# Kernel optimization log

Measured on AMD Instinct MI355X. Metric: run time of the kernel, lower is better.

Reference implementation:

```python
import jax, jax.numpy as jnp
import numpy as np

N = 200000  # number of mesh nodes (source hardcodes n; scaled to production)

def setup_inputs() -> dict:
    key = jax.random.key(0)
    ks = jax.random.split(key, 7)
    spatial = jax.random.normal(ks[0], (N, 64), dtype=jnp.float32)
    structural = jax.random.normal(ks[1], (N, 131), dtype=jnp.float32)
    neighbour = jax.random.randint(ks[2], (N, 3), 0, N, dtype=jnp.int64)
    # Conv1d(kernel_size=1) == linear layer; weights [out_c, in_c]
    Wc = jax.random.normal(ks[3], (256, 195), dtype=jnp.float32) * (1.0 / np.sqrt(195))
    bc = jax.random.normal(ks[4], (256,), dtype=jnp.float32) * 0.01
    Wa = jax.random.normal(ks[5], (256, 131), dtype=jnp.float32) * (1.0 / np.sqrt(131))
    ba = jax.random.normal(ks[6], (256,), dtype=jnp.float32) * 0.01
    return {"spatial": spatial, "structural": structural, "neighbour": neighbour,
            "Wc": Wc, "bc": bc, "Wa": Wa, "ba": ba}

def reference(spatial, structural, neighbour, Wc, bc, Wa, ba):
    # Combination1: concat(spatial[n,64], structural[n,131]) -> 1x1 conv (linear)
    a1 = jnp.concatenate([spatial, structural], axis=1)      # [n,195]
    out1 = jnp.einsum('nc,oc->no', a1, Wc) + bc               # [n,256]
    # Aggregation1: mean of self + 3 gathered neighbor feature vectors
    nbr_feats = structural[neighbour]                          # [n,3,131] gather
    vec4 = (structural + nbr_feats.sum(axis=1)) * 0.25        # [n,131]
    out2 = jnp.einsum('nc,oc->no', vec4, Wa) + ba             # [n,256]
    return (out1, out2)
```

## Files before the change

kernel.cpp:

```cpp
#include <hip/hip_runtime.h>
#include <hip/hip_bf16.h>

#define K1 195
#define K1P 224
#define K2 131
#define K2P 160
#define OC 256
#define BM 32
#define S1 232
#define S2 168
#define SO 260
#define THREADS 512

typedef __attribute__((ext_vector_type(4))) float f32x4;
typedef __attribute__((ext_vector_type(8))) short bf16x8;
typedef __attribute__((ext_vector_type(4))) short bf16x4;

__device__ __forceinline__ short f2b(float x) {
    __hip_bfloat16 h = __float2bfloat16(x);
    return *reinterpret_cast<short*>(&h);
}

__global__ void prep_weights_v14(const float* __restrict__ Wc, const float* __restrict__ Wa,
                                 __hip_bfloat16* __restrict__ WcP, __hip_bfloat16* __restrict__ WaP) {
    int t = blockIdx.x * blockDim.x + threadIdx.x;
    const int total1 = OC * K1P;
    const int total2 = OC * K2P;
    if (t < total1) {
        int oc = t / K1P, k = t - oc * K1P;
        float v = (k < K1) ? Wc[oc * K1 + k] : 0.0f;
        WcP[t] = __float2bfloat16(v);
    } else if (t < total1 + total2) {
        int u = t - total1;
        int oc = u / K2P, k = u - oc * K2P;
        float v = (k < K2) ? Wa[oc * K2 + k] : 0.0f;
        WaP[u] = __float2bfloat16(v);
    }
}

__global__ __launch_bounds__(THREADS) void fused_mesh_v14(
        const float* __restrict__ spatial,
        const float* __restrict__ structural,
        const int* __restrict__ neighbour,
        const __hip_bfloat16* __restrict__ WcP,
        const float* __restrict__ bc,
        const __hip_bfloat16* __restrict__ WaP,
        const float* __restrict__ ba,
        float* __restrict__ out1,
        float* __restrict__ out2,
        int n) {
    __shared__ union SMem {
        struct {
            short A1[BM][S1];
            short A2[BM][S2];
            int   nidx[BM * 3];
        } s;
        float ols[BM][SO];
    } smem;

    const int t = threadIdx.x;
    const int r0 = blockIdx.x * BM;

    if (t < BM * 3) {
        size_t gi = (size_t)r0 * 3 + t;
        smem.s.nidx[t] = (gi < (size_t)n * 3) ? neighbour[gi] : 0;
    }

    for (int e = t; e < BM * (K1P - K1); e += THREADS) {
        int r = e / (K1P - K1);
        int k = K1 + (e - r * (K1P - K1));
        smem.s.A1[r][k] = 0;
    }
    for (int e = t; e < BM * (K2P - K2); e += THREADS) {
        int r = e / (K2P - K2);
        int k = K2 + (e - r * (K2P - K2));
        smem.s.A2[r][k] = 0;
    }

    {
        int r  = t >> 4;
        int c0 = (t & 15) * 4;
        int rr = min(r0 + r, n - 1);
        f32x4 v = *(const f32x4*)(spatial + (size_t)rr * 64 + c0);
        bf16x4 o;
        #pragma unroll
        for (int j = 0; j < 4; ++j) o[j] = f2b(v[j]);
        *(bf16x4*)&smem.s.A1[r][c0] = o;
    }
    __syncthreads();

    for (int e = t; e < BM * K2; e += THREADS) {
        int r = e / K2;
        int k = e - r * K2;
        int rr = min(r0 + r, n - 1);
        float self = structural[(size_t)rr * K2 + k];
        int n0 = smem.s.nidx[r * 3 + 0];
        int n1 = smem.s.nidx[r * 3 + 1];
        int n2 = smem.s.nidx[r * 3 + 2];
        float v = self + structural[(size_t)n0 * K2 + k]
                       + structural[(size_t)n1 * K2 + k]
                       + structural[(size_t)n2 * K2 + k];
        smem.s.A1[r][64 + k] = f2b(self);
        smem.s.A2[r][k]      = f2b(v * 0.25f);
    }
    __syncthreads();

    const int wid  = t >> 6;
    const int lane = t & 63;
    const int lr   = lane & 15;
    const int lkc  = lane >> 4;
    const int colBase = wid * 32;

    f32x4 acc1[2][2], acc2[2][2];
    #pragma unroll
    for (int i = 0; i < 2; ++i)
        #pragma unroll
        for (int j = 0; j < 2; ++j) {
            acc1[i][j] = (f32x4){0.f, 0.f, 0.f, 0.f};
            acc2[i][j] = (f32x4){0.f, 0.f, 0.f, 0.f};
        }

    #pragma unroll
    for (int ks = 0; ks < K1P; ks += 32) {
        bf16x8 a[2], b[2];
        #pragma unroll
        for (int rt = 0; rt < 2; ++rt)
            a[rt] = *(const bf16x8*)&smem.s.A1[rt * 16 + lr][ks + lkc * 8];
        #pragma unroll
        for (int ct = 0; ct < 2; ++ct) {
            int oc = colBase + ct * 16 + lr;
            b[ct] = *(const bf16x8*)(WcP + (size_t)oc * K1P + ks + lkc * 8);
        }
        #pragma unroll
        for (int rt = 0; rt < 2; ++rt)
            #pragma unroll
            for (int ct = 0; ct < 2; ++ct)
                acc1[ct][rt] = __builtin_amdgcn_mfma_f32_16x16x32_bf16(b[ct], a[rt], acc1[ct][rt], 0, 0, 0);
    }

    #pragma unroll
    for (int ks = 0; ks < K2P; ks += 32) {
        bf16x8 a[2], b[2];
        #pragma unroll
        for (int rt = 0; rt < 2; ++rt)
            a[rt] = *(const bf16x8*)&smem.s.A2[rt * 16 + lr][ks + lkc * 8];
        #pragma unroll
        for (int ct = 0; ct < 2; ++ct) {
            int oc = colBase + ct * 16 + lr;
            b[ct] = *(const bf16x8*)(WaP + (size_t)oc * K2P + ks + lkc * 8);
        }
        #pragma unroll
        for (int rt = 0; rt < 2; ++rt)
            #pragma unroll
            for (int ct = 0; ct < 2; ++ct)
                acc2[ct][rt] = __builtin_amdgcn_mfma_f32_16x16x32_bf16(b[ct], a[rt], acc2[ct][rt], 0, 0, 0);
    }

    __syncthreads();

    #pragma unroll
    for (int ct = 0; ct < 2; ++ct) {
        int oc0 = colBase + ct * 16 + lkc * 4;
        f32x4 b4 = *(const f32x4*)(bc + oc0);
        #pragma unroll
        for (int rt = 0; rt < 2; ++rt)
            *(f32x4*)&smem.ols[rt * 16 + lr][oc0] = acc1[ct][rt] + b4;
    }
    __syncthreads();
    #pragma unroll
    for (int i = 0; i < 4; ++i) {
        int row = wid * 4 + i;
        f32x4 v = *(const f32x4*)&smem.ols[row][lane * 4];
        int node = r0 + row;
        if (node < n)
            __builtin_nontemporal_store(v, (f32x4*)(out1 + (size_t)node * OC + lane * 4));
    }
    __syncthreads();

    #pragma unroll
    for (int ct = 0; ct < 2; ++ct) {
        int oc0 = colBase + ct * 16 + lkc * 4;
        f32x4 b4 = *(const f32x4*)(ba + oc0);
        #pragma unroll
        for (int rt = 0; rt < 2; ++rt)
            *(f32x4*)&smem.ols[rt * 16 + lr][oc0] = acc2[ct][rt] + b4;
    }
    __syncthreads();
    #pragma unroll
    for (int i = 0; i < 4; ++i) {
        int row = wid * 4 + i;
        f32x4 v = *(const f32x4*)&smem.ols[row][lane * 4];
        int node = r0 + row;
        if (node < n)
            __builtin_nontemporal_store(v, (f32x4*)(out2 + (size_t)node * OC + lane * 4));
    }
}

extern "C" void kernel_launch(void* const* d_in, const int* in_sizes, int n_in,
                              void* d_out, int out_size, void* d_ws, size_t ws_size,
                              hipStream_t stream) {
    const float* spatial    = (const float*)d_in[0];
    const float* structural = (const float*)d_in[1];
    const int*   neighbour  = (const int*)d_in[2];
    const float* Wc = (const float*)d_in[3];
    const float* bc = (const float*)d_in[4];
    const float* Wa = (const float*)d_in[5];
    const float* ba = (const float*)d_in[6];

    const int n = in_sizes[0] / 64;

    float* out1 = (float*)d_out;
    float* out2 = out1 + (size_t)n * OC;

    __hip_bfloat16* WcP = (__hip_bfloat16*)d_ws;
    __hip_bfloat16* WaP = WcP + OC * K1P;

    {
        const int total = OC * K1P + OC * K2P;
        prep_weights_v14<<<(total + 255) / 256, 256, 0, stream>>>(Wc, Wa, WcP, WaP);
    }
    {
        const int grid = (n + BM - 1) / BM;
        fused_mesh_v14<<<grid, THREADS, 0, stream>>>(spatial, structural, neighbour,
                                                     WcP, bc, WaP, ba, out1, out2, n);
    }
}
```

Before: 181.8 us.

## Pre-convert structural features to padded bf16 table for cheaper neighbour gathers

Adds a pre-pass that converts the structural array to a bf16 table padded to 136 columns in workspace. The fused kernel then gathers self and neighbour rows as 16-byte bf16x8 vector loads instead of scalar fp32 loads, halving gather bytes and allowing vectorised access. The cost is an extra full pass over structural (read fp32, write bf16) and neighbour sums built from bf16-rounded values, a small accuracy change. The new path runs only if the workspace is large enough; otherwise the old path is kept.

```diff
diff --git a/kernel.cpp b/kernel.cpp
--- a/kernel.cpp
+++ b/kernel.cpp
@@ -4,6 +4,7 @@
 #define K1 195
 #define K1P 224
 #define K2 131
+#define K2B 136
 #define K2P 160
 #define OC 256
 #define BM 32
@@ -15,13 +16,17 @@
 typedef __attribute__((ext_vector_type(4))) float f32x4;
 typedef __attribute__((ext_vector_type(8))) short bf16x8;
 typedef __attribute__((ext_vector_type(4))) short bf16x4;
+typedef __attribute__((ext_vector_type(2))) short bf16x2;
 
 __device__ __forceinline__ short f2b(float x) {
     __hip_bfloat16 h = __float2bfloat16(x);
     return *reinterpret_cast<short*>(&h);
 }
-
-__global__ void prep_weights_v14(const float* __restrict__ Wc, const float* __restrict__ Wa,
+__device__ __forceinline__ float b2f(short x) {
+    return __uint_as_float(((unsigned)(unsigned short)x) << 16);
+}
+
+__global__ void prep_weights_v15(const float* __restrict__ Wc, const float* __restrict__ Wa,
                                  __hip_bfloat16* __restrict__ WcP, __hip_bfloat16* __restrict__ WaP) {
     int t = blockIdx.x * blockDim.x + threadIdx.x;
     const int total1 = OC * K1P;
@@ -38,9 +43,26 @@
     }
 }
 
-__global__ __launch_bounds__(THREADS) void fused_mesh_v14(
+__global__ void prep_structB_v15(const float* __restrict__ structural,
+                                 __hip_bfloat16* __restrict__ structB, int n) {
+    int idx = blockIdx.x * blockDim.x + threadIdx.x;
+    const int ppr = K2B / 2;
+    if (idx >= n * ppr) return;
+    int r = idx / ppr;
+    int c = (idx - r * ppr) * 2;
+    float v0 = (c     < K2) ? structural[(size_t)r * K2 + c]     : 0.0f;
+    float v1 = (c + 1 < K2) ? structural[(size_t)r * K2 + c + 1] : 0.0f;
+    bf16x2 o;
+    o[0] = f2b(v0);
+    o[1] = f2b(v1);
+    *(bf16x2*)((short*)structB + (size_t)r * K2B + c) = o;
+}
+
+template<bool USE_SB>
+__global__ __launch_bounds__(THREADS) void fused_mesh_v15(
         const float* __restrict__ spatial,
         const float* __restrict__ structural,
+        const __hip_bfloat16* __restrict__ structB,
         const int* __restrict__ neighbour,
         const __hip_bfloat16* __restrict__ WcP,
         const float* __restrict__ bc,
@@ -89,19 +111,41 @@
     }
     __syncthreads();
 
-    for (int e = t; e < BM * K2; e += THREADS) {
-        int r = e / K2;
-        int k = e - r * K2;
-        int rr = min(r0 + r, n - 1);
-        float self = structural[(size_t)rr * K2 + k];
-        int n0 = smem.s.nidx[r * 3 + 0];
-        int n1 = smem.s.nidx[r * 3 + 1];
-        int n2 = smem.s.nidx[r * 3 + 2];
-        float v = self + structural[(size_t)n0 * K2 + k]
-                       + structural[(size_t)n1 * K2 + k]
-                       + structural[(size_t)n2 * K2 + k];
-        smem.s.A1[r][64 + k] = f2b(self);
-        smem.s.A2[r][k]      = f2b(v * 0.25f);
+    if constexpr (USE_SB) {
+        for (int u = t; u < BM * 17; u += THREADS) {
+            int r = u / 17;
+            int c = (u - r * 17) * 8;
+            int rr = min(r0 + r, n - 1);
+            const short* sb = (const short*)structB;
+            bf16x8 vs = *(const bf16x8*)(sb + (size_t)rr * K2B + c);
+            *(bf16x8*)&smem.s.A1[r][64 + c] = vs;
+            int n0 = smem.s.nidx[r * 3 + 0];
+            int n1 = smem.s.nidx[r * 3 + 1];
+            int n2 = smem.s.nidx[r * 3 + 2];
+            bf16x8 v0 = *(const bf16x8*)(sb + (size_t)n0 * K2B + c);
+            bf16x8 v1 = *(const bf16x8*)(sb + (size_t)n1 * K2B + c);
+            bf16x8 v2 = *(const bf16x8*)(sb + (size_t)n2 * K2B + c);
+            bf16x8 o;
+            #pragma unroll
+            for (int j = 0; j < 8; ++j)
+                o[j] = f2b((b2f(vs[j]) + b2f(v0[j]) + b2f(v1[j]) + b2f(v2[j])) * 0.25f);
+            *(bf16x8*)&smem.s.A2[r][c] = o;
+        }
+    } else {
+        for (int e = t; e < BM * K2; e += THREADS) {
+            int r = e / K2;
+            int k = e - r * K2;
+            int rr = min(r0 + r, n - 1);
+            float self = structural[(size_t)rr * K2 + k];
+            int n0 = smem.s.nidx[r * 3 + 0];
+            int n1 = smem.s.nidx[r * 3 + 1];
+            int n2 = smem.s.nidx[r * 3 + 2];
+            float v = self + structural[(size_t)n0 * K2 + k]
+                           + structural[(size_t)n1 * K2 + k]
+                           + structural[(size_t)n2 * K2 + k];
+            smem.s.A1[r][64 + k] = f2b(self);
+            smem.s.A2[r][k]      = f2b(v * 0.25f);
+        }
     }
     __syncthreads();
 
@@ -215,13 +259,23 @@
     __hip_bfloat16* WcP = (__hip_bfloat16*)d_ws;
     __hip_bfloat16* WaP = WcP + OC * K1P;
 
+    const size_t wbytes = (size_t)(OC * K1P + OC * K2P) * sizeof(__hip_bfloat16);
+    const size_t sbytes = (size_t)n * K2B * sizeof(__hip_bfloat16);
+    const bool use_sb = (ws_size >= wbytes + sbytes);
+    __hip_bfloat16* structB = (__hip_bfloat16*)((char*)d_ws + wbytes);
+
     {
         const int total = OC * K1P + OC * K2P;
-        prep_weights_v14<<<(total + 255) / 256, 256, 0, stream>>>(Wc, Wa, WcP, WaP);
-    }
-    {
-        const int grid = (n + BM - 1) / BM;
-        fused_mesh_v14<<<grid, THREADS, 0, stream>>>(spatial, structural, neighbour,
-                                                     WcP, bc, WaP, ba, out1, out2, n);
-    }
-}
+        prep_weights_v15<<<(total + 255) / 256, 256, 0, stream>>>(Wc, Wa, WcP, WaP);
+    }
+    const int grid = (n + BM - 1) / BM;
+    if (use_sb) {
+        const int totalp = n * (K2B / 2);
+        prep_structB_v15<<<(totalp + 255) / 256, 256, 0, stream>>>(structural, structB, n);
+        fused_mesh_v15<true><<<grid, THREADS, 0, stream>>>(spatial, structural, structB, neighbour,
+                                                           WcP, bc, WaP, ba, out1, out2, n);
+    } else {
+        fused_mesh_v15<false><<<grid, THREADS, 0, stream>>>(spatial, structural, structB, neighbour,
+                                                            WcP, bc, WaP, ba, out1, out2, n);
+    }
+}
```

Result: no change. 183.2 us (+0.8%).
